# Performance work log

Hardware: AMD Instinct MI355X
Metric: run time of the kernel (lower is better)

## Reference

```python
import jax, jax.numpy as jnp
import numpy as np

L = 128          # lifted_dim
NS = 50000       # source nodes
NT = 50000       # target nodes
E = 640000       # edges
SLOPE = 0.01     # cfg.leaky_slope (torch LeakyReLU default)
EPS = 1e-5       # BatchNorm eps


def _glorot(key, shape):
    fan_in, fan_out = shape[0], shape[1]
    lim = np.sqrt(6.0 / (fan_in + fan_out)).astype(np.float32)
    return jax.random.uniform(key, shape, jnp.float32, -lim, lim)


def setup_inputs() -> dict:
    key = jax.random.key(0)
    ks = jax.random.split(key, 16)
    x_s = jax.random.normal(ks[0], (NS, L), jnp.float32)
    x_t = jax.random.normal(ks[1], (NT, L), jnp.float32)
    edge_index = jax.random.randint(ks[2], (2, E), 0, NT, jnp.int64)
    edge_attr = jax.random.normal(ks[3], (E, L), jnp.float32)
    x_u = jax.random.normal(ks[4], (L,), jnp.float32)
    M = 2 * L  # message_dim
    U = 4 * L  # update_dim
    params = {
        'W1': _glorot(ks[5], (M, M)), 'b1': jnp.zeros((M,), jnp.float32),
        'W2': _glorot(ks[6], (M, M)), 'b2': jnp.zeros((M,), jnp.float32),
        'U1': _glorot(ks[7], (U, U)), 'c1': jnp.zeros((U,), jnp.float32),
        'U2': _glorot(ks[8], (U, L)), 'c2': jnp.zeros((L,), jnp.float32),
        'gamma': jnp.ones((L,), jnp.float32), 'beta': jnp.zeros((L,), jnp.float32),
    }
    return dict(x_s=x_s, x_t=x_t, edge_index=edge_index, edge_attr=edge_attr, x_u=x_u, **params)


def reference(x_s, x_t, edge_index, edge_attr, x_u,
              W1, b1, W2, b2, U1, c1, U2, c2, gamma, beta):
    src, tgt = edge_index[0], edge_index[1]
    # edge messages: gather source features + edge attrs -> 2-layer MLP
    msg = jnp.concatenate([x_s[src], edge_attr], axis=1)          # [E, 2L]
    msg = jax.nn.leaky_relu(msg @ W1 + b1, negative_slope=SLOPE)
    msg = msg @ W2 + b2                                           # [E, 2L]
    # scatter-add aggregation onto target nodes
    agg = jax.ops.segment_sum(msg, tgt, num_segments=x_t.shape[0])  # [NT, 2L]
    # node update
    xu = jnp.broadcast_to(x_u[None, :], (x_t.shape[0], x_u.shape[0]))
    h = jnp.concatenate([x_t, agg, xu], axis=-1)                  # [NT, 4L]
    h = jax.nn.leaky_relu(h @ U1 + c1, negative_slope=SLOPE)
    h = h @ U2 + c2                                               # [NT, L]
    # BatchNorm1d (training mode: batch statistics, biased variance)
    mu = jnp.mean(h, axis=0)
    var = jnp.var(h, axis=0)
    return gamma * (h - mu) * jax.lax.rsqrt(var + EPS) + beta
```

## Files before the change

### kernel.cpp

```cpp
#include <hip/hip_runtime.h>

typedef unsigned int u32;
typedef unsigned short u16;
typedef __attribute__((ext_vector_type(8))) short short8;
typedef __attribute__((ext_vector_type(8))) unsigned short ushort8v;
typedef __attribute__((ext_vector_type(4))) unsigned short ushort4v;
typedef __attribute__((ext_vector_type(4))) float f32x4;

#define NSRC 50000
#define NTGT 50000
#define NEDGE 640000
#define LDIM 128
#define SLOPE 0.01f

#define MFMA(a, b, c) __builtin_amdgcn_mfma_f32_16x16x32_bf16((a), (b), (c), 0, 0, 0)

__device__ __forceinline__ u16 f2bf(float f) {
  union { float f; u32 u; } v; v.f = f;
  u32 r = v.u + 0x7FFFu + ((v.u >> 16) & 1u);
  return (u16)(r >> 16);
}
__device__ __forceinline__ float bf2f(u16 h) {
  union { u32 u; float f; } v; v.u = ((u32)h) << 16; return v.f;
}

__device__ __forceinline__ void pack_one(const float* __restrict__ src, u16* __restrict__ dst,
                                         int N, int kc, int cb, int lane) {
  int quad = lane >> 4, l16 = lane & 15;
  const float* s = src + (size_t)(kc * 32 + quad * 8) * N + cb * 16 + l16;
  u16* o = dst + ((size_t)(kc * (N / 16) + cb) * 64 + lane) * 8;
  ushort8v p;
#pragma unroll
  for (int j = 0; j < 8; ++j) p[j] = f2bf(s[(size_t)j * N]);
  *(ushort8v*)o = p;
}

__global__ void k_prep(const float* __restrict__ W1, const float* __restrict__ W2,
                       const float* __restrict__ U1, const float* __restrict__ U2,
                       u16* __restrict__ w1p, u16* __restrict__ w2p,
                       u16* __restrict__ u1p, u16* __restrict__ u2p) {
  int id = blockIdx.x * 256 + threadIdx.x;
  if (id < 8192) {
    int l = id, lane = l & 63, g = l >> 6;
    pack_one(W1, w1p, 256, g >> 4, g & 15, lane);
  } else if (id < 16384) {
    int l = id - 8192, lane = l & 63, g = l >> 6;
    pack_one(W2, w2p, 256, g >> 4, g & 15, lane);
  } else if (id < 49152) {
    int l = id - 16384, lane = l & 63, g = l >> 6;
    pack_one(U1, u1p, 512, g >> 5, g & 31, lane);
  } else if (id < 57344) {
    int l = id - 49152, lane = l & 63, g = l >> 6;
    pack_one(U2, u2p, 128, g >> 3, g & 7, lane);
  }
}

__global__ void k_count(const int* __restrict__ tgt, int* __restrict__ cnt,
                        int* __restrict__ rank) {
  int e = blockIdx.x * 256 + threadIdx.x;
  if (e < NEDGE) rank[e] = atomicAdd(&cnt[tgt[e]], 1);
}

__global__ void k_scan(const int* __restrict__ cnt, int* __restrict__ rowstart) {
  __shared__ int part[1024];
  int tid = threadIdx.x;
  int base = tid * 49;
  int s = 0;
  for (int i = 0; i < 49; ++i) { int idx = base + i; if (idx < NTGT) s += cnt[idx]; }
  part[tid] = s;
  __syncthreads();
  for (int off = 1; off < 1024; off <<= 1) {
    int v = (tid >= off) ? part[tid - off] : 0;
    __syncthreads();
    part[tid] += v;
    __syncthreads();
  }
  int run = (tid > 0) ? part[tid - 1] : 0;
  for (int i = 0; i < 49; ++i) {
    int idx = base + i;
    if (idx < NTGT) { rowstart[idx] = run; run += cnt[idx]; }
  }
  if (tid == 1023) rowstart[NTGT] = part[1023];
}

__global__ void k_pos(const int* __restrict__ tgt, const int* __restrict__ rowstart,
                      int* __restrict__ pos) {
  int e = blockIdx.x * 256 + threadIdx.x;
  if (e < NEDGE) pos[e] = rowstart[tgt[e]] + pos[e];
}

__global__ __launch_bounds__(256, 4) void k_edge(
    const float* __restrict__ xs, const int* __restrict__ srcp,
    const float* __restrict__ ea,
    const u16* __restrict__ w1p, const u16* __restrict__ w2p,
    const float* __restrict__ b1, const float* __restrict__ b2,
    const int* __restrict__ pos, u16* __restrict__ msg) {
  __shared__ u16 tile[64][264];
  const int tid = threadIdx.x;
  const int ebase = blockIdx.x * 64;

  {
    const int et = tid >> 2, p = tid & 3;
    const float* srow;
    if (p < 2) {
      int sidx = srcp[ebase + et];
      srow = xs + (size_t)sidx * LDIM + p * 64;
    } else {
      srow = ea + (size_t)(ebase + et) * LDIM + (p - 2) * 64;
    }
    const float4* f4 = (const float4*)srow;
    u16* dst = &tile[et][p * 64];
#pragma unroll
    for (int i = 0; i < 8; ++i) {
      float4 a = f4[2 * i], b = f4[2 * i + 1];
      ushort8v pk = { f2bf(a.x), f2bf(a.y), f2bf(a.z), f2bf(a.w),
                      f2bf(b.x), f2bf(b.y), f2bf(b.z), f2bf(b.w) };
      *(ushort8v*)(dst + i * 8) = pk;
    }
  }
  __syncthreads();

  const int lane = tid & 63, wid = tid >> 6;
  const int quad = lane >> 4, l16 = lane & 15;
  const int colb = wid * 64;
  const short8* __restrict__ w1f = (const short8*)w1p;
  const short8* __restrict__ w2f = (const short8*)w2p;

  f32x4 acc[4][4];
#pragma unroll
  for (int a = 0; a < 4; ++a)
#pragma unroll
    for (int b = 0; b < 4; ++b) acc[a][b] = (f32x4){0.f, 0.f, 0.f, 0.f};

#pragma unroll 2
  for (int kc = 0; kc < 8; ++kc) {
    short8 af[4], bfr[4];
#pragma unroll
    for (int ct = 0; ct < 4; ++ct)
      bfr[ct] = w1f[(size_t)(kc * 16 + wid * 4 + ct) * 64 + lane];
#pragma unroll
    for (int rt = 0; rt < 4; ++rt)
      af[rt] = *(const short8*)&tile[rt * 16 + l16][kc * 32 + quad * 8];
#pragma unroll
    for (int rt = 0; rt < 4; ++rt)
#pragma unroll
      for (int ct = 0; ct < 4; ++ct)
        acc[rt][ct] = MFMA(af[rt], bfr[ct], acc[rt][ct]);
  }
  __syncthreads();
#pragma unroll
  for (int ct = 0; ct < 4; ++ct) {
    int col = colb + ct * 16 + l16;
    float bias = b1[col];
#pragma unroll
    for (int rt = 0; rt < 4; ++rt)
#pragma unroll
      for (int r = 0; r < 4; ++r) {
        int row = rt * 16 + quad * 4 + r;
        float v = acc[rt][ct][r] + bias;
        v = v > 0.f ? v : SLOPE * v;
        tile[row][col] = f2bf(v);
      }
  }
  __syncthreads();

#pragma unroll
  for (int a = 0; a < 4; ++a)
#pragma unroll
    for (int b = 0; b < 4; ++b) acc[a][b] = (f32x4){0.f, 0.f, 0.f, 0.f};
#pragma unroll 2
  for (int kc = 0; kc < 8; ++kc) {
    short8 af[4], bfr[4];
#pragma unroll
    for (int ct = 0; ct < 4; ++ct)
      bfr[ct] = w2f[(size_t)(kc * 16 + wid * 4 + ct) * 64 + lane];
#pragma unroll
    for (int rt = 0; rt < 4; ++rt)
      af[rt] = *(const short8*)&tile[rt * 16 + l16][kc * 32 + quad * 8];
#pragma unroll
    for (int rt = 0; rt < 4; ++rt)
#pragma unroll
      for (int ct = 0; ct < 4; ++ct)
        acc[rt][ct] = MFMA(af[rt], bfr[ct], acc[rt][ct]);
  }
  __syncthreads();
#pragma unroll
  for (int ct = 0; ct < 4; ++ct) {
    int col = colb + ct * 16 + l16;
    float bias = b2[col];
#pragma unroll
    for (int rt = 0; rt < 4; ++rt)
#pragma unroll
      for (int r = 0; r < 4; ++r) {
        int row = rt * 16 + quad * 4 + r;
        tile[row][col] = f2bf(acc[rt][ct][r] + bias);
      }
  }
  __syncthreads();

  {
    const int et = tid >> 2, p = tid & 3;
    const int gp = pos[ebase + et];
    u16* dst = msg + (size_t)gp * 256 + p * 64;
    const u16* sl = &tile[et][p * 64];
#pragma unroll
    for (int i = 0; i < 8; ++i)
      *(ushort8v*)(dst + i * 8) = *(const ushort8v*)(sl + i * 8);
  }
}

__global__ __launch_bounds__(256, 4) void k_node(
    const float* __restrict__ xt, const float* __restrict__ xu,
    const u16* __restrict__ msg, const int* __restrict__ rowstart,
    const u16* __restrict__ u1p, const u16* __restrict__ u2p,
    const float* __restrict__ c1, const float* __restrict__ c2,
    float* __restrict__ h2, float* __restrict__ stats) {
  __shared__ u16 ain[32][520];
  const int tid = threadIdx.x;
  const int lane = tid & 63, wid = tid >> 6;
  const int quad = lane >> 4, l16 = lane & 15;
  const int tbase = blockIdx.x * 32;

  for (int s = wid; s < 32; s += 4) {
    int t = tbase + s;
    if (t < NTGT) {
      {
        float4 v; int col;
        if (lane < 32) { v = ((const float4*)(xt + (size_t)t * LDIM))[lane]; col = lane * 4; }
        else           { v = ((const float4*)xu)[lane - 32]; col = 384 + (lane - 32) * 4; }
        ushort4v p = { f2bf(v.x), f2bf(v.y), f2bf(v.z), f2bf(v.w) };
        *(ushort4v*)&ain[s][col] = p;
      }
      int rs = rowstart[t], re = rowstart[t + 1];
      float acc8[8] = {0.f, 0.f, 0.f, 0.f, 0.f, 0.f, 0.f, 0.f};
      const u16* mb = msg + ((size_t)rs + (lane >> 5)) * 256 + (lane & 31) * 8;
      int n = re - rs, nfull = n & ~1;
      for (int r = 0; r < nfull; r += 2) {
        ushort8v m = *(const ushort8v*)(mb + (size_t)r * 256);
#pragma unroll
        for (int j = 0; j < 8; ++j) acc8[j] += bf2f(m[j]);
      }
      if (n & 1) {
        if (lane < 32) {
          ushort8v m = *(const ushort8v*)(msg + (size_t)(re - 1) * 256 + lane * 8);
#pragma unroll
          for (int j = 0; j < 8; ++j) acc8[j] += bf2f(m[j]);
        }
      }
#pragma unroll
      for (int j = 0; j < 8; ++j) acc8[j] += __shfl_down(acc8[j], 32);
      if (lane < 32) {
        ushort8v p;
#pragma unroll
        for (int j = 0; j < 8; ++j) p[j] = f2bf(acc8[j]);
        *(ushort8v*)&ain[s][128 + lane * 8] = p;
      }
    } else {
      ushort8v z = {0, 0, 0, 0, 0, 0, 0, 0};
      *(ushort8v*)&ain[s][lane * 8] = z;
    }
  }
  __syncthreads();

  const short8* __restrict__ u1f = (const short8*)u1p;
  const short8* __restrict__ u2f = (const short8*)u2p;

  f32x4 acc[2][2][4];
#pragma unroll
  for (int h = 0; h < 2; ++h)
#pragma unroll
    for (int a = 0; a < 2; ++a)
#pragma unroll
      for (int b = 0; b < 4; ++b) acc[h][a][b] = (f32x4){0.f, 0.f, 0.f, 0.f};

#pragma unroll 2
  for (int kc = 0; kc < 16; ++kc) {
    short8 af[2];
#pragma unroll
    for (int rt = 0; rt < 2; ++rt)
      af[rt] = *(const short8*)&ain[rt * 16 + l16][kc * 32 + quad * 8];
#pragma unroll
    for (int h = 0; h < 2; ++h) {
      short8 bfr[4];
#pragma unroll
      for (int ct = 0; ct < 4; ++ct)
        bfr[ct] = u1f[(size_t)(kc * 32 + h * 16 + wid * 4 + ct) * 64 + lane];
#pragma unroll
      for (int rt = 0; rt < 2; ++rt)
#pragma unroll
        for (int ct = 0; ct < 4; ++ct)
          acc[h][rt][ct] = MFMA(af[rt], bfr[ct], acc[h][rt][ct]);
    }
  }
  __syncthreads();
#pragma unroll
  for (int h = 0; h < 2; ++h)
#pragma unroll
    for (int ct = 0; ct < 4; ++ct) {
      int col = h * 256 + wid * 64 + ct * 16 + l16;
      float cb = c1[col];
#pragma unroll
      for (int rt = 0; rt < 2; ++rt)
#pragma unroll
        for (int r = 0; r < 4; ++r) {
          int row = rt * 16 + quad * 4 + r;
          float v = acc[h][rt][ct][r] + cb;
          v = v > 0.f ? v : SLOPE * v;
          ain[row][col] = f2bf(v);
        }
    }
  __syncthreads();

  const int colb2 = wid * 32;
  f32x4 acc2[2][2];
#pragma unroll
  for (int a = 0; a < 2; ++a)
#pragma unroll
    for (int b = 0; b < 2; ++b) acc2[a][b] = (f32x4){0.f, 0.f, 0.f, 0.f};
#pragma unroll 4
  for (int kc = 0; kc < 16; ++kc) {
    short8 af[2], bfr[2];
#pragma unroll
    for (int ct = 0; ct < 2; ++ct)
      bfr[ct] = u2f[(size_t)(kc * 8 + wid * 2 + ct) * 64 + lane];
#pragma unroll
    for (int rt = 0; rt < 2; ++rt)
      af[rt] = *(const short8*)&ain[rt * 16 + l16][kc * 32 + quad * 8];
#pragma unroll
    for (int rt = 0; rt < 2; ++rt)
#pragma unroll
      for (int ct = 0; ct < 2; ++ct)
        acc2[rt][ct] = MFMA(af[rt], bfr[ct], acc2[rt][ct]);
  }
  float s1[2] = {0.f, 0.f}, s2[2] = {0.f, 0.f};
#pragma unroll
  for (int ct = 0; ct < 2; ++ct) {
    int col = colb2 + ct * 16 + l16;
    float cb = c2[col];
#pragma unroll
    for (int rt = 0; rt < 2; ++rt)
#pragma unroll
      for (int r = 0; r < 4; ++r) {
        int row = rt * 16 + quad * 4 + r;
        int t = tbase + row;
        if (t < NTGT) {
          float v = acc2[rt][ct][r] + cb;
          h2[(size_t)t * LDIM + col] = v;
          s1[ct] += v; s2[ct] += v * v;
        }
      }
  }
#pragma unroll
  for (int ct = 0; ct < 2; ++ct) {
    float a = s1[ct], b = s2[ct];
    a += __shfl_down(a, 32); b += __shfl_down(b, 32);
    a += __shfl_down(a, 16); b += __shfl_down(b, 16);
    if (lane < 16) {
      atomicAdd(&stats[colb2 + ct * 16 + l16], a);
      atomicAdd(&stats[128 + colb2 + ct * 16 + l16], b);
    }
  }
}

__global__ void k_bnfin(const float* __restrict__ stats, const float* __restrict__ gamma,
                        const float* __restrict__ beta, float* __restrict__ ss) {
  int c = threadIdx.x;
  if (c < 128) {
    float mu = stats[c] * (1.0f / NTGT);
    float var = stats[128 + c] * (1.0f / NTGT) - mu * mu;
    float rs = rsqrtf(var + 1e-5f);
    float sc = gamma[c] * rs;
    ss[c] = sc;
    ss[128 + c] = beta[c] - mu * sc;
  }
}

__global__ void k_bnapply(const float* __restrict__ h2, const float* __restrict__ ss,
                          float* __restrict__ out) {
  int i = blockIdx.x * 256 + threadIdx.x;
  const int total = NTGT * LDIM / 4;
  const float4* h4 = (const float4*)h2;
  const float4* sc4 = (const float4*)ss;
  const float4* sh4 = (const float4*)(ss + 128);
  float4* o4 = (float4*)out;
  for (; i < total; i += gridDim.x * 256) {
    int cg = i & 31;
    float4 h = h4[i], sc = sc4[cg], sh = sh4[cg];
    float4 r = { h.x * sc.x + sh.x, h.y * sc.y + sh.y,
                 h.z * sc.z + sh.z, h.w * sc.w + sh.w };
    o4[i] = r;
  }
}

extern "C" void kernel_launch(void* const* d_in, const int* in_sizes, int n_in,
                              void* d_out, int out_size, void* d_ws, size_t ws_size,
                              hipStream_t stream) {
  (void)in_sizes; (void)n_in; (void)out_size; (void)ws_size;
  const float* xs    = (const float*)d_in[0];
  const float* xt    = (const float*)d_in[1];
  const int*   ei    = (const int*)d_in[2];
  const float* ea    = (const float*)d_in[3];
  const float* xu    = (const float*)d_in[4];
  const float* W1    = (const float*)d_in[5];
  const float* b1    = (const float*)d_in[6];
  const float* W2    = (const float*)d_in[7];
  const float* b2    = (const float*)d_in[8];
  const float* U1    = (const float*)d_in[9];
  const float* c1    = (const float*)d_in[10];
  const float* U2    = (const float*)d_in[11];
  const float* c2    = (const float*)d_in[12];
  const float* gamma = (const float*)d_in[13];
  const float* beta  = (const float*)d_in[14];

  char* ws = (char*)d_ws;
  u16* w1p   = (u16*)(ws + 0x000000);
  u16* w2p   = (u16*)(ws + 0x020000);
  u16* u1p   = (u16*)(ws + 0x040000);
  u16* u2p   = (u16*)(ws + 0x0C0000);
  int* cnt   = (int*)(ws + 0x0E0000);
  int* rowst = (int*)(ws + 0x120000);
  int* pos   = (int*)(ws + 0x160000);
  float* stats = (float*)(ws + 0x400000);
  float* ss    = stats + 256;
  float* h2  = (float*)(ws + 0x410000);
  u16* msg   = (u16*)(ws + 0x1C80000);

  const int* srcp = ei;
  const int* tgtp = ei + NEDGE;

  hipMemsetAsync(cnt, 0, NTGT * 4, stream);
  hipMemsetAsync(stats, 0, 256 * 4, stream);
  k_prep<<<224, 256, 0, stream>>>(W1, W2, U1, U2, w1p, w2p, u1p, u2p);
  k_count<<<2500, 256, 0, stream>>>(tgtp, cnt, pos);
  k_scan<<<1, 1024, 0, stream>>>(cnt, rowst);
  k_pos<<<2500, 256, 0, stream>>>(tgtp, rowst, pos);
  k_edge<<<10000, 256, 0, stream>>>(xs, srcp, ea, w1p, w2p, b1, b2, pos, msg);
  k_node<<<1563, 256, 0, stream>>>(xt, xu, msg, rowst, u1p, u2p, c1, c2, h2, stats);
  k_bnfin<<<1, 128, 0, stream>>>(stats, gamma, beta, ss);
  k_bnapply<<<6250, 256, 0, stream>>>(h2, ss, (float*)d_out);
}
```

Baseline: 1.005 ms.

## Fold W2 into U1 and precompute per-source W1 projection before edge gather

The second edge-MLP layer is linear, so W2 is multiplied into the agg rows of U1 (W2·U1_agg). The b2 contribution becomes a degree-scaled bias, and the constant x_u block becomes an extra bias. The edge kernel then runs only one 128-deep GEMM on edge_attr plus a gathered per-source projection x_s·W1_top, which a separate node-level GEMM computes once per source. This removes one edge GEMM and halves the other, at the cost of more bf16 rounding from the composed weights and an extra pass that writes and gathers a bf16 P buffer.

```diff
diff --git a/kernel.cpp b/kernel.cpp
--- a/kernel.cpp
+++ b/kernel.cpp
@@ -24,34 +24,79 @@
   union { u32 u; float f; } v; v.u = ((u32)h) << 16; return v.f;
 }
 
-__device__ __forceinline__ void pack_one(const float* __restrict__ src, u16* __restrict__ dst,
-                                         int N, int kc, int cb, int lane) {
-  int quad = lane >> 4, l16 = lane & 15;
-  const float* s = src + (size_t)(kc * 32 + quad * 8) * N + cb * 16 + l16;
-  u16* o = dst + ((size_t)(kc * (N / 16) + cb) * 64 + lane) * 8;
-  ushort8v p;
-#pragma unroll
-  for (int j = 0; j < 8; ++j) p[j] = f2bf(s[(size_t)j * N]);
-  *(ushort8v*)o = p;
-}
-
-__global__ void k_prep(const float* __restrict__ W1, const float* __restrict__ W2,
-                       const float* __restrict__ U1, const float* __restrict__ U2,
-                       u16* __restrict__ w1p, u16* __restrict__ w2p,
-                       u16* __restrict__ u1p, u16* __restrict__ u2p) {
+__global__ void k_w2b(const float* __restrict__ W2, const float* __restrict__ U1,
+                      float* __restrict__ w2b) {
+  const int i = blockIdx.x;
+  const int j = threadIdx.x;
+  const float* __restrict__ u = U1 + (size_t)128 * 512;
+  float a0 = 0.f, a1 = 0.f;
+#pragma unroll 8
+  for (int k = 0; k < 256; ++k) {
+    float w = W2[(size_t)i * 256 + k];
+    a0 += w * u[(size_t)k * 512 + j];
+    a1 += w * u[(size_t)k * 512 + j + 256];
+  }
+  w2b[(size_t)i * 512 + j] = a0;
+  w2b[(size_t)i * 512 + j + 256] = a1;
+}
+
+__global__ void k_bias(const float* __restrict__ U1, const float* __restrict__ xu,
+                       const float* __restrict__ b2, const float* __restrict__ c1,
+                       float* __restrict__ c1e, float* __restrict__ vb) {
+  const int j = threadIdx.x;
+  float s = c1[j];
+#pragma unroll 4
+  for (int k = 0; k < 128; ++k) s += xu[k] * U1[(size_t)(384 + k) * 512 + j];
+  float v = 0.f;
+#pragma unroll 4
+  for (int k = 0; k < 256; ++k) v += b2[k] * U1[(size_t)(128 + k) * 512 + j];
+  c1e[j] = s;
+  vb[j] = v;
+}
+
+__global__ void k_prep(const float* __restrict__ W1, const float* __restrict__ U1,
+                       const float* __restrict__ U2, const float* __restrict__ w2b,
+                       u16* __restrict__ w1a, u16* __restrict__ w1b,
+                       u16* __restrict__ u1e, u16* __restrict__ u2p) {
   int id = blockIdx.x * 256 + threadIdx.x;
-  if (id < 8192) {
-    int l = id, lane = l & 63, g = l >> 6;
-    pack_one(W1, w1p, 256, g >> 4, g & 15, lane);
-  } else if (id < 16384) {
-    int l = id - 8192, lane = l & 63, g = l >> 6;
-    pack_one(W2, w2p, 256, g >> 4, g & 15, lane);
-  } else if (id < 49152) {
-    int l = id - 16384, lane = l & 63, g = l >> 6;
-    pack_one(U1, u1p, 512, g >> 5, g & 31, lane);
-  } else if (id < 57344) {
-    int l = id - 49152, lane = l & 63, g = l >> 6;
-    pack_one(U2, u2p, 128, g >> 3, g & 7, lane);
+  int lane = id & 63, quad = (lane >> 4), l16 = lane & 15;
+  if (id < 4096) {
+    int g = id >> 6;
+    int kc = g >> 4, cb = g & 15;
+    const float* s = W1 + (size_t)(kc * 32 + quad * 8) * 256 + cb * 16 + l16;
+    ushort8v p;
+#pragma unroll
+    for (int j = 0; j < 8; ++j) p[j] = f2bf(s[(size_t)j * 256]);
+    *(ushort8v*)(w1a + ((size_t)g * 64 + lane) * 8) = p;
+  } else if (id < 8192) {
+    int g = (id - 4096) >> 6;
+    int kc = g >> 4, cb = g & 15;
+    const float* s = W1 + (size_t)(128 + kc * 32 + quad * 8) * 256 + cb * 16 + l16;
+    ushort8v p;
+#pragma unroll
+    for (int j = 0; j < 8; ++j) p[j] = f2bf(s[(size_t)j * 256]);
+    *(ushort8v*)(w1b + ((size_t)g * 64 + lane) * 8) = p;
+  } else if (id < 32768) {
+    int g = (id - 8192) >> 6;
+    int kc = g >> 5, cb = g & 31;
+    int col = cb * 16 + l16;
+    ushort8v p;
+#pragma unroll
+    for (int j = 0; j < 8; ++j) {
+      int row = kc * 32 + quad * 8 + j;
+      float v = (row < 128) ? U1[(size_t)row * 512 + col]
+                            : w2b[(size_t)(row - 128) * 512 + col];
+      p[j] = f2bf(v);
+    }
+    *(ushort8v*)(u1e + ((size_t)g * 64 + lane) * 8) = p;
+  } else if (id < 40960) {
+    int g = (id - 32768) >> 6;
+    int kc = g >> 3, cb = g & 7;
+    const float* s = U2 + (size_t)(kc * 32 + quad * 8) * 128 + cb * 16 + l16;
+    ushort8v p;
+#pragma unroll
+    for (int j = 0; j < 8; ++j) p[j] = f2bf(s[(size_t)j * 128]);
+    *(ushort8v*)(u2p + ((size_t)g * 64 + lane) * 8) = p;
   }
 }
 
@@ -89,33 +134,30 @@
   if (e < NEDGE) pos[e] = rowstart[tgt[e]] + pos[e];
 }
 
-__global__ __launch_bounds__(256, 4) void k_edge(
-    const float* __restrict__ xs, const int* __restrict__ srcp,
-    const float* __restrict__ ea,
-    const u16* __restrict__ w1p, const u16* __restrict__ w2p,
-    const float* __restrict__ b1, const float* __restrict__ b2,
-    const int* __restrict__ pos, u16* __restrict__ msg) {
-  __shared__ u16 tile[64][264];
+__global__ __launch_bounds__(256, 3) void k_pgemm(
+    const float* __restrict__ xs, const u16* __restrict__ w1ap,
+    const float* __restrict__ b1, u16* __restrict__ P) {
+  __shared__ u16 At[64][136];
+  __shared__ u16 Ot[64][264];
   const int tid = threadIdx.x;
-  const int ebase = blockIdx.x * 64;
-
+  const int base = blockIdx.x * 64;
   {
     const int et = tid >> 2, p = tid & 3;
-    const float* srow;
-    if (p < 2) {
-      int sidx = srcp[ebase + et];
-      srow = xs + (size_t)sidx * LDIM + p * 64;
+    const int row = base + et;
+    u16* dst = &At[et][p * 32];
+    if (row < NSRC) {
+      const float4* f4 = (const float4*)(xs + (size_t)row * LDIM + p * 32);
+#pragma unroll
+      for (int i = 0; i < 4; ++i) {
+        float4 a = f4[2 * i], b = f4[2 * i + 1];
+        ushort8v pk = { f2bf(a.x), f2bf(a.y), f2bf(a.z), f2bf(a.w),
+                        f2bf(b.x), f2bf(b.y), f2bf(b.z), f2bf(b.w) };
+        *(ushort8v*)(dst + i * 8) = pk;
+      }
     } else {
-      srow = ea + (size_t)(ebase + et) * LDIM + (p - 2) * 64;
-    }
-    const float4* f4 = (const float4*)srow;
-    u16* dst = &tile[et][p * 64];
-#pragma unroll
-    for (int i = 0; i < 8; ++i) {
-      float4 a = f4[2 * i], b = f4[2 * i + 1];
-      ushort8v pk = { f2bf(a.x), f2bf(a.y), f2bf(a.z), f2bf(a.w),
-                      f2bf(b.x), f2bf(b.y), f2bf(b.z), f2bf(b.w) };
-      *(ushort8v*)(dst + i * 8) = pk;
+      ushort8v z = {0, 0, 0, 0, 0, 0, 0, 0};
+#pragma unroll
+      for (int i = 0; i < 4; ++i) *(ushort8v*)(dst + i * 8) = z;
     }
   }
   __syncthreads();
@@ -123,31 +165,28 @@
   const int lane = tid & 63, wid = tid >> 6;
   const int quad = lane >> 4, l16 = lane & 15;
   const int colb = wid * 64;
-  const short8* __restrict__ w1f = (const short8*)w1p;
-  const short8* __restrict__ w2f = (const short8*)w2p;
+  const short8* __restrict__ wf = (const short8*)w1ap;
 
   f32x4 acc[4][4];
 #pragma unroll
   for (int a = 0; a < 4; ++a)
 #pragma unroll
     for (int b = 0; b < 4; ++b) acc[a][b] = (f32x4){0.f, 0.f, 0.f, 0.f};
-
-#pragma unroll 2
-  for (int kc = 0; kc < 8; ++kc) {
+#pragma unroll
+  for (int kc = 0; kc < 4; ++kc) {
     short8 af[4], bfr[4];
 #pragma unroll
     for (int ct = 0; ct < 4; ++ct)
-      bfr[ct] = w1f[(size_t)(kc * 16 + wid * 4 + ct) * 64 + lane];
+      bfr[ct] = wf[(size_t)(kc * 16 + wid * 4 + ct) * 64 + lane];
 #pragma unroll
     for (int rt = 0; rt < 4; ++rt)
-      af[rt] = *(const short8*)&tile[rt * 16 + l16][kc * 32 + quad * 8];
+      af[rt] = *(const short8*)&At[rt * 16 + l16][kc * 32 + quad * 8];
 #pragma unroll
     for (int rt = 0; rt < 4; ++rt)
 #pragma unroll
       for (int ct = 0; ct < 4; ++ct)
         acc[rt][ct] = MFMA(af[rt], bfr[ct], acc[rt][ct]);
   }
-  __syncthreads();
 #pragma unroll
   for (int ct = 0; ct < 4; ++ct) {
     int col = colb + ct * 16 + l16;
@@ -157,43 +196,90 @@
 #pragma unroll
       for (int r = 0; r < 4; ++r) {
         int row = rt * 16 + quad * 4 + r;
-        float v = acc[rt][ct][r] + bias;
-        v = v > 0.f ? v : SLOPE * v;
-        tile[row][col] = f2bf(v);
-      }
-  }
-  __syncthreads();
-
+        Ot[row][col] = f2bf(acc[rt][ct][r] + bias);
+      }
+  }
+  __syncthreads();
+  {
+    const int et = tid >> 2, p = tid & 3;
+    const int row = base + et;
+    if (row < NSRC) {
+      u16* dst = P + (size_t)row * 256 + p * 64;
+      const u16* sl = &Ot[et][p * 64];
+#pragma unroll
+      for (int i = 0; i < 8; ++i)
+        *(ushort8v*)(dst + i * 8) = *(const ushort8v*)(sl + i * 8);
+    }
+  }
+}
+
+__global__ __launch_bounds__(256, 3) void k_edge(
+    const float* __restrict__ ea, const int* __restrict__ srcp,
+    const u16* __restrict__ Pg, const u16* __restrict__ w1bp,
+    const int* __restrict__ pos, u16* __restrict__ tbuf) {
+  __shared__ u16 At[64][136];
+  __shared__ u16 Pt[64][264];
+  const int tid = threadIdx.x;
+  const int ebase = blockIdx.x * 64;
+
+  {
+    const int et = tid >> 2, p = tid & 3;
+    if (p < 2) {
+      const float4* f4 = (const float4*)(ea + (size_t)(ebase + et) * LDIM + p * 64);
+      u16* dst = &At[et][p * 64];
+#pragma unroll
+      for (int i = 0; i < 8; ++i) {
+        float4 a = f4[2 * i], b = f4[2 * i + 1];
+        ushort8v pk = { f2bf(a.x), f2bf(a.y), f2bf(a.z), f2bf(a.w),
+                        f2bf(b.x), f2bf(b.y), f2bf(b.z), f2bf(b.w) };
+        *(ushort8v*)(dst + i * 8) = pk;
+      }
+    } else {
+      int sidx = srcp[ebase + et];
+      const ushort8v* pr = (const ushort8v*)(Pg + (size_t)sidx * 256 + (p - 2) * 128);
+      u16* dst = &Pt[et][(p - 2) * 128];
+#pragma unroll
+      for (int i = 0; i < 16; ++i) *(ushort8v*)(dst + i * 8) = pr[i];
+    }
+  }
+  __syncthreads();
+
+  const int lane = tid & 63, wid = tid >> 6;
+  const int quad = lane >> 4, l16 = lane & 15;
+  const int colb = wid * 64;
+  const short8* __restrict__ wf = (const short8*)w1bp;
+
+  f32x4 acc[4][4];
 #pragma unroll
   for (int a = 0; a < 4; ++a)
 #pragma unroll
     for (int b = 0; b < 4; ++b) acc[a][b] = (f32x4){0.f, 0.f, 0.f, 0.f};
-#pragma unroll 2
-  for (int kc = 0; kc < 8; ++kc) {
+#pragma unroll
+  for (int kc = 0; kc < 4; ++kc) {
     short8 af[4], bfr[4];
 #pragma unroll
     for (int ct = 0; ct < 4; ++ct)
-      bfr[ct] = w2f[(size_t)(kc * 16 + wid * 4 + ct) * 64 + lane];
+      bfr[ct] = wf[(size_t)(kc * 16 + wid * 4 + ct) * 64 + lane];
 #pragma unroll
     for (int rt = 0; rt < 4; ++rt)
-      af[rt] = *(const short8*)&tile[rt * 16 + l16][kc * 32 + quad * 8];
+      af[rt] = *(const short8*)&At[rt * 16 + l16][kc * 32 + quad * 8];
 #pragma unroll
     for (int rt = 0; rt < 4; ++rt)
 #pragma unroll
       for (int ct = 0; ct < 4; ++ct)
         acc[rt][ct] = MFMA(af[rt], bfr[ct], acc[rt][ct]);
   }
-  __syncthreads();
 #pragma unroll
   for (int ct = 0; ct < 4; ++ct) {
     int col = colb + ct * 16 + l16;
-    float bias = b2[col];
 #pragma unroll
     for (int rt = 0; rt < 4; ++rt)
 #pragma unroll
       for (int r = 0; r < 4; ++r) {
         int row = rt * 16 + quad * 4 + r;
-        tile[row][col] = f2bf(acc[rt][ct][r] + bias);
+        float v = acc[rt][ct][r] + bf2f(Pt[row][col]);
+        v = v > 0.f ? v : SLOPE * v;
+        Pt[row][col] = f2bf(v);
       }
   }
   __syncthreads();
@@ -201,8 +287,8 @@
   {
     const int et = tid >> 2, p = tid & 3;
     const int gp = pos[ebase + et];
-    u16* dst = msg + (size_t)gp * 256 + p * 64;
-    const u16* sl = &tile[et][p * 64];
+    u16* dst = tbuf + (size_t)gp * 256 + p * 64;
+    const u16* sl = &Pt[et][p * 64];
 #pragma unroll
     for (int i = 0; i < 8; ++i)
       *(ushort8v*)(dst + i * 8) = *(const ushort8v*)(sl + i * 8);
@@ -210,12 +296,13 @@
 }
 
 __global__ __launch_bounds__(256, 4) void k_node(
-    const float* __restrict__ xt, const float* __restrict__ xu,
-    const u16* __restrict__ msg, const int* __restrict__ rowstart,
-    const u16* __restrict__ u1p, const u16* __restrict__ u2p,
-    const float* __restrict__ c1, const float* __restrict__ c2,
+    const float* __restrict__ xt, const u16* __restrict__ tbuf,
+    const int* __restrict__ rowstart, const u16* __restrict__ u1e,
+    const u16* __restrict__ u2p, const float* __restrict__ c1e,
+    const float* __restrict__ vb, const float* __restrict__ c2,
     float* __restrict__ h2, float* __restrict__ stats) {
   __shared__ u16 ain[32][520];
+  __shared__ float sdeg[32];
   const int tid = threadIdx.x;
   const int lane = tid & 63, wid = tid >> 6;
   const int quad = lane >> 4, l16 = lane & 15;
@@ -224,16 +311,15 @@
   for (int s = wid; s < 32; s += 4) {
     int t = tbase + s;
     if (t < NTGT) {
-      {
-        float4 v; int col;
-        if (lane < 32) { v = ((const float4*)(xt + (size_t)t * LDIM))[lane]; col = lane * 4; }
-        else           { v = ((const float4*)xu)[lane - 32]; col = 384 + (lane - 32) * 4; }
+      if (lane < 32) {
+        float4 v = ((const float4*)(xt + (size_t)t * LDIM))[lane];
         ushort4v p = { f2bf(v.x), f2bf(v.y), f2bf(v.z), f2bf(v.w) };
-        *(ushort4v*)&ain[s][col] = p;
+        *(ushort4v*)&ain[s][lane * 4] = p;
       }
       int rs = rowstart[t], re = rowstart[t + 1];
+      if (lane == 0) sdeg[s] = (float)(re - rs);
       float acc8[8] = {0.f, 0.f, 0.f, 0.f, 0.f, 0.f, 0.f, 0.f};
-      const u16* mb = msg + ((size_t)rs + (lane >> 5)) * 256 + (lane & 31) * 8;
+      const u16* mb = tbuf + ((size_t)rs + (lane >> 5)) * 256 + (lane & 31) * 8;
       int n = re - rs, nfull = n & ~1;
       for (int r = 0; r < nfull; r += 2) {
         ushort8v m = *(const ushort8v*)(mb + (size_t)r * 256);
@@ -242,7 +328,7 @@
       }
       if (n & 1) {
         if (lane < 32) {
-          ushort8v m = *(const ushort8v*)(msg + (size_t)(re - 1) * 256 + lane * 8);
+          ushort8v m = *(const ushort8v*)(tbuf + (size_t)(re - 1) * 256 + lane * 8);
 #pragma unroll
           for (int j = 0; j < 8; ++j) acc8[j] += bf2f(m[j]);
         }
@@ -258,11 +344,12 @@
     } else {
       ushort8v z = {0, 0, 0, 0, 0, 0, 0, 0};
       *(ushort8v*)&ain[s][lane * 8] = z;
-    }
-  }
-  __syncthreads();
-
-  const short8* __restrict__ u1f = (const short8*)u1p;
+      if (lane == 0) sdeg[s] = 0.f;
+    }
+  }
+  __syncthreads();
+
+  const short8* __restrict__ u1f = (const short8*)u1e;
   const short8* __restrict__ u2f = (const short8*)u2p;
 
   f32x4 acc[2][2][4];
@@ -274,7 +361,7 @@
       for (int b = 0; b < 4; ++b) acc[h][a][b] = (f32x4){0.f, 0.f, 0.f, 0.f};
 
 #pragma unroll 2
-  for (int kc = 0; kc < 16; ++kc) {
+  for (int kc = 0; kc < 12; ++kc) {
     short8 af[2];
 #pragma unroll
     for (int rt = 0; rt < 2; ++rt)
@@ -298,13 +385,13 @@
 #pragma unroll
     for (int ct = 0; ct < 4; ++ct) {
       int col = h * 256 + wid * 64 + ct * 16 + l16;
-      float cb = c1[col];
+      float cb = c1e[col], vbb = vb[col];
 #pragma unroll
       for (int rt = 0; rt < 2; ++rt)
 #pragma unroll
         for (int r = 0; r < 4; ++r) {
           int row = rt * 16 + quad * 4 + r;
-          float v = acc[h][rt][ct][r] + cb;
+          float v = acc[h][rt][ct][r] + cb + sdeg[row] * vbb;
           v = v > 0.f ? v : SLOPE * v;
           ain[row][col] = f2bf(v);
         }
@@ -413,29 +500,36 @@
   const float* beta  = (const float*)d_in[14];
 
   char* ws = (char*)d_ws;
-  u16* w1p   = (u16*)(ws + 0x000000);
-  u16* w2p   = (u16*)(ws + 0x020000);
-  u16* u1p   = (u16*)(ws + 0x040000);
-  u16* u2p   = (u16*)(ws + 0x0C0000);
-  int* cnt   = (int*)(ws + 0x0E0000);
-  int* rowst = (int*)(ws + 0x120000);
-  int* pos   = (int*)(ws + 0x160000);
-  float* stats = (float*)(ws + 0x400000);
+  u16* w1a   = (u16*)(ws + 0x000000);
+  u16* w1b   = (u16*)(ws + 0x010000);
+  u16* u1e   = (u16*)(ws + 0x020000);
+  u16* u2p   = (u16*)(ws + 0x080000);
+  float* w2b = (float*)(ws + 0x0A0000);
+  float* c1e = (float*)(ws + 0x120000);
+  float* vbv = (float*)(ws + 0x120800);
+  int* cnt   = (int*)(ws + 0x130000);
+  int* rowst = (int*)(ws + 0x161000);
+  int* pos   = (int*)(ws + 0x192000);
+  float* stats = (float*)(ws + 0x410000);
   float* ss    = stats + 256;
-  float* h2  = (float*)(ws + 0x410000);
-  u16* msg   = (u16*)(ws + 0x1C80000);
+  u16*   Pbuf = (u16*)(ws + 0x412000);
+  float* h2   = (float*)(ws + 0x412000);
+  u16*   tbuf = (u16*)(ws + 0x1C80000);
 
   const int* srcp = ei;
   const int* tgtp = ei + NEDGE;
 
   hipMemsetAsync(cnt, 0, NTGT * 4, stream);
   hipMemsetAsync(stats, 0, 256 * 4, stream);
-  k_prep<<<224, 256, 0, stream>>>(W1, W2, U1, U2, w1p, w2p, u1p, u2p);
+  k_w2b<<<256, 256, 0, stream>>>(W2, U1, w2b);
+  k_bias<<<1, 512, 0, stream>>>(U1, xu, b2, c1, c1e, vbv);
+  k_prep<<<160, 256, 0, stream>>>(W1, U1, U2, w2b, w1a, w1b, u1e, u2p);
   k_count<<<2500, 256, 0, stream>>>(tgtp, cnt, pos);
   k_scan<<<1, 1024, 0, stream>>>(cnt, rowst);
   k_pos<<<2500, 256, 0, stream>>>(tgtp, rowst, pos);
-  k_edge<<<10000, 256, 0, stream>>>(xs, srcp, ea, w1p, w2p, b1, b2, pos, msg);
-  k_node<<<1563, 256, 0, stream>>>(xt, xu, msg, rowst, u1p, u2p, c1, c2, h2, stats);
+  k_pgemm<<<782, 256, 0, stream>>>(xs, w1a, b1, Pbuf);
+  k_edge<<<10000, 256, 0, stream>>>(ea, srcp, Pbuf, w1b, pos, tbuf);
+  k_node<<<1563, 256, 0, stream>>>(xt, tbuf, rowst, u1e, u2p, c1e, vbv, c2, h2, stats);
   k_bnfin<<<1, 128, 0, stream>>>(stats, gamma, beta, ss);
   k_bnapply<<<6250, 256, 0, stream>>>(h2, ss, (float*)d_out);
 }
```

New measurement: 974.1 us. -3.1%, faster.
